# Kernel optimization log

Hardware: AMD Instinct MI355X
Metric: run time of the kernel (lower is better)

Reference implementation:

```python
import math
import jax, jax.numpy as jnp
import numpy as np

DIM = 1536
HEADS = 8
DK = 64
DV = 192
NRPF = 192  # num_rel_pos_features, divisible by 6
SEQ = 1536
BATCH = 4
SCALE = DK ** -0.5


def get_positional_embed(n, feature_size):
    # distances in [-(n-1), n-1], length 2n-1
    dist = jnp.arange(-n + 1, n).astype(jnp.float32)
    adist = jnp.abs(dist)[:, None]  # [2n-1, 1]
    f = feature_size // 6  # 3 feature fns, each doubled by sign channel
    # exponential half-life features
    max_range = math.log(n) / math.log(2.0)
    half_life = 2.0 ** jnp.linspace(3.0, max_range, f)[None, :]
    emb_exp = jnp.exp(-math.log(2.0) / half_life * adist)
    # central mask features
    center_widths = (2.0 ** jnp.arange(1, f + 1).astype(jnp.float32) - 1.0)[None, :]
    emb_cm = (center_widths > adist).astype(jnp.float32)
    # gamma pdf features
    stddev = n / (2.0 * f)
    start_mean = n / float(f)
    mean = jnp.linspace(start_mean, float(n), f)[None, :]
    conc = (mean / stddev) ** 2
    rate = mean / stddev ** 2
    log_unnorm = (conc - 1.0) * jnp.log(jnp.maximum(adist, 1e-20)) - rate * adist
    log_norm = jax.scipy.special.gammaln(conc) - conc * jnp.log(rate)
    prob = jnp.exp(log_unnorm - log_norm) + 1e-8
    emb_g = prob / jnp.max(prob, axis=-1, keepdims=True)
    emb = jnp.concatenate([emb_exp, emb_cm, emb_g], axis=-1)  # [2n-1, feat/2]
    return jnp.concatenate([emb, jnp.sign(dist)[:, None] * emb], axis=-1)  # [2n-1, feat]


def relative_shift(x):
    # x: [b, h, n, 2n-1] -> [b, h, n, n] via the Transformer-XL shift trick
    b, h, t1, t2 = x.shape
    x = jnp.concatenate([jnp.zeros_like(x[..., :1]), x], axis=-1)  # [b,h,t1,t2+1]
    x = x.reshape(b, h, t2 + 1, t1)[:, :, 1:, :].reshape(b, h, t1, t2)
    return x[..., : (t2 + 2) // 2]


def layer_norm(x, g, b, eps=1e-5):
    mu = jnp.mean(x, axis=-1, keepdims=True)
    var = jnp.var(x, axis=-1, keepdims=True)
    return (x - mu) * jax.lax.rsqrt(var + eps) * g + b


def setup_inputs() -> dict:
    key = jax.random.key(0)
    ks = jax.random.split(key, 16)
    d, h, dk, dv = DIM, HEADS, DK, DV
    inp = {
        "x": jax.random.normal(ks[0], (BATCH, SEQ, d), dtype=jnp.float32),
        "ln1_g": jnp.ones((d,), jnp.float32),
        "ln1_b": jnp.zeros((d,), jnp.float32),
        "Wq": jax.random.normal(ks[1], (d, h * dk), jnp.float32) / math.sqrt(d),
        "Wk": jax.random.normal(ks[2], (d, h * dk), jnp.float32) / math.sqrt(d),
        "Wv": jax.random.normal(ks[3], (d, h * dv), jnp.float32) / math.sqrt(d),
        "Wo": jax.random.normal(ks[4], (h * dv, d), jnp.float32) / math.sqrt(h * dv),
        "bo": jnp.zeros((d,), jnp.float32),
        "Wrk": jax.random.normal(ks[5], (NRPF, h * dk), jnp.float32) / math.sqrt(NRPF),
        "rel_content_bias": jax.random.normal(ks[6], (1, h, 1, dk), jnp.float32),
        "rel_pos_bias": jax.random.normal(ks[7], (1, h, 1, dk), jnp.float32),
        "ln2_g": jnp.ones((d,), jnp.float32),
        "ln2_b": jnp.zeros((d,), jnp.float32),
        "W1": jax.random.normal(ks[8], (d, 2 * d), jnp.float32) / math.sqrt(d),
        "b1": jnp.zeros((2 * d,), jnp.float32),
        "W2": jax.random.normal(ks[9], (2 * d, d), jnp.float32) / math.sqrt(2 * d),
        "b2": jnp.zeros((d,), jnp.float32),
    }
    return inp


def _attention(x, Wq, Wk, Wv, Wo, bo, Wrk, rel_content_bias, rel_pos_bias):
    b, n, _ = x.shape
    h, dk, dv = HEADS, DK, DV
    q = (x @ Wq).reshape(b, n, h, dk).transpose(0, 2, 1, 3) * SCALE  # [b,h,n,dk]
    k = (x @ Wk).reshape(b, n, h, dk).transpose(0, 2, 1, 3)
    v = (x @ Wv).reshape(b, n, h, dv).transpose(0, 2, 1, 3)
    content_logits = jnp.einsum('bhid,bhjd->bhij', q + rel_content_bias, k)
    positions = get_positional_embed(n, NRPF)  # [2n-1, NRPF]
    rel_k = (positions @ Wrk).reshape(2 * n - 1, h, dk).transpose(1, 0, 2)  # [h,2n-1,dk]
    rel_logits = jnp.einsum('bhid,hjd->bhij', q + rel_pos_bias, rel_k)
    rel_logits = relative_shift(rel_logits)  # [b,h,n,n]
    attn = jax.nn.softmax(content_logits + rel_logits, axis=-1)
    out = jnp.einsum('bhij,bhjd->bhid', attn, v)
    out = out.transpose(0, 2, 1, 3).reshape(b, n, h * dv)
    return out @ Wo + bo


def reference(x, ln1_g, ln1_b, Wq, Wk, Wv, Wo, bo, Wrk, rel_content_bias,
              rel_pos_bias, ln2_g, ln2_b, W1, b1, W2, b2):
    # pre-LN attention with residual
    x = x + _attention(layer_norm(x, ln1_g, ln1_b), Wq, Wk, Wv, Wo, bo, Wrk,
                       rel_content_bias, rel_pos_bias)
    # MLP block (carries its own LayerNorm and residual)
    y = layer_norm(x, ln2_g, ln2_b)
    y = jax.nn.relu(y @ W1 + b1)
    y = y @ W2 + b2
    return y + x
```

## Files before the change

kernel.cpp:

```cpp
#include <hip/hip_runtime.h>
#include <hip/hip_bf16.h>
#include <math.h>

#define SEQN 1536
#define NH 8
#define MROWS 6144
#define NDIST 3071

typedef __attribute__((ext_vector_type(8))) _Float16 f16x8;
typedef __attribute__((ext_vector_type(4))) _Float16 f16x4;
typedef __attribute__((ext_vector_type(4))) float f32x4;

#define MFMAH(a, b, c) __builtin_amdgcn_mfma_f32_16x16x32_f16(a, b, c, 0, 0, 0)

__device__ __forceinline__ void gl_lds16(const void* g, void* l) {
  __builtin_amdgcn_global_load_lds(
      (const __attribute__((address_space(1))) void*)g,
      (__attribute__((address_space(3))) void*)l, 16, 0, 0);
}

__global__ __launch_bounds__(64) void pos_embed_kernel(float* __restrict__ pos) {
  int row = blockIdx.x;
  int j = threadIdx.x;
  if (j >= 32) return;
  float dist = (float)(row - (SEQN - 1));
  float adist = fabsf(dist);
  float sgn = (dist > 0.f) ? 1.f : (dist < 0.f ? -1.f : 0.f);

  const float max_range = 10.58496250072116f;
  float hl = exp2f(3.0f + ((max_range - 3.0f) / 31.0f) * (float)j);
  float e_exp = expf(-0.6931471805599453f / hl * adist);

  float cw = exp2f((float)(j + 1)) - 1.0f;
  float e_cm = (cw > adist) ? 1.0f : 0.0f;

  float mean = 48.0f * (float)(j + 1);
  float tt = mean / 24.0f;
  float conc = tt * tt;
  float rate = mean / 576.0f;
  float log_unnorm = (conc - 1.0f) * logf(fmaxf(adist, 1e-20f)) - rate * adist;
  float log_norm = lgammaf(conc) - conc * logf(rate);
  float prob = expf(log_unnorm - log_norm) + 1e-8f;
  float mx = prob;
  #pragma unroll
  for (int off = 16; off >= 1; off >>= 1)
    mx = fmaxf(mx, __shfl_xor(mx, off, 32));
  float e_g = prob / mx;

  float* o = pos + (size_t)row * 192;
  o[j] = e_exp;        o[32 + j] = e_cm;        o[64 + j] = e_g;
  o[96 + j] = sgn * e_exp; o[128 + j] = sgn * e_cm; o[160 + j] = sgn * e_g;
}

__global__ __launch_bounds__(512) void relk_kernel(
    const float* __restrict__ pos, const float* __restrict__ Wrk,
    const float* __restrict__ pb, _Float16* __restrict__ rk, float* __restrict__ PR) {
  __shared__ float prow[16][192];
  const int d0 = blockIdx.x * 16;
  const int t = threadIdx.x;
  #pragma unroll
  for (int p = 0; p < 6; ++p) {
    int idx = t + p * 512;
    int r = idx / 192, c = idx - r * 192;
    prow[r][c] = pos[(size_t)(d0 + r) * 192 + c];
  }
  __syncthreads();
  float acc[16];
  #pragma unroll
  for (int r = 0; r < 16; ++r) acc[r] = 0.f;
  #pragma unroll 4
  for (int kk = 0; kk < 192; ++kk) {
    float wv = Wrk[(size_t)kk * 512 + t];
    #pragma unroll
    for (int r = 0; r < 16; ++r) acc[r] = fmaf(prow[r][kk], wv, acc[r]);
  }
  #pragma unroll
  for (int r = 0; r < 16; ++r)
    rk[(size_t)(d0 + r) * 512 + t] = (_Float16)acc[r];
  float pbv = pb[t];
  #pragma unroll
  for (int r = 0; r < 16; ++r) {
    float pv = pbv * acc[r];
    #pragma unroll
    for (int off = 32; off >= 1; off >>= 1) pv += __shfl_xor(pv, off);
    if ((t & 63) == 0 && (d0 + r) < NDIST)
      PR[(size_t)(t >> 6) * NDIST + d0 + r] = pv;
  }
}

__global__ __launch_bounds__(256) void ln_kernel(
    const float* __restrict__ x, const float* __restrict__ g,
    const float* __restrict__ bta, _Float16* __restrict__ oh) {
  const int row = blockIdx.x;
  const int t = threadIdx.x;
  __shared__ float red[4];
  __shared__ float bc[2];
  const float4* xr = (const float4*)(x + (size_t)row * 1536);
  float4 v0 = xr[t];
  float4 v1 = make_float4(0.f, 0.f, 0.f, 0.f);
  if (t < 128) v1 = xr[256 + t];
  float s = v0.x + v0.y + v0.z + v0.w;
  if (t < 128) s += v1.x + v1.y + v1.z + v1.w;
  #pragma unroll
  for (int off = 32; off >= 1; off >>= 1) s += __shfl_xor(s, off);
  if ((t & 63) == 0) red[t >> 6] = s;
  __syncthreads();
  if (t == 0) bc[0] = (red[0] + red[1] + red[2] + red[3]) * (1.f / 1536.f);
  __syncthreads();
  const float mu = bc[0];
  float d, s2 = 0.f;
  d = v0.x - mu; s2 += d * d; d = v0.y - mu; s2 += d * d;
  d = v0.z - mu; s2 += d * d; d = v0.w - mu; s2 += d * d;
  if (t < 128) {
    d = v1.x - mu; s2 += d * d; d = v1.y - mu; s2 += d * d;
    d = v1.z - mu; s2 += d * d; d = v1.w - mu; s2 += d * d;
  }
  #pragma unroll
  for (int off = 32; off >= 1; off >>= 1) s2 += __shfl_xor(s2, off);
  if ((t & 63) == 0) red[t >> 6] = s2;
  __syncthreads();
  if (t == 0) bc[1] = (red[0] + red[1] + red[2] + red[3]) * (1.f / 1536.f);
  __syncthreads();
  const float inv = rsqrtf(bc[1] + 1e-5f);
  const float4* g4 = (const float4*)g;
  const float4* b4 = (const float4*)bta;
  float4 gg = g4[t], bb = b4[t];
  f16x4 hv;
  hv[0] = (_Float16)((v0.x - mu) * inv * gg.x + bb.x);
  hv[1] = (_Float16)((v0.y - mu) * inv * gg.y + bb.y);
  hv[2] = (_Float16)((v0.z - mu) * inv * gg.z + bb.z);
  hv[3] = (_Float16)((v0.w - mu) * inv * gg.w + bb.w);
  *(f16x4*)(oh + (size_t)row * 1536 + t * 4) = hv;
  if (t < 128) {
    gg = g4[256 + t]; bb = b4[256 + t];
    hv[0] = (_Float16)((v1.x - mu) * inv * gg.x + bb.x);
    hv[1] = (_Float16)((v1.y - mu) * inv * gg.y + bb.y);
    hv[2] = (_Float16)((v1.z - mu) * inv * gg.z + bb.z);
    hv[3] = (_Float16)((v1.w - mu) * inv * gg.w + bb.w);
    *(f16x4*)(oh + (size_t)row * 1536 + 1024 + t * 4) = hv;
  }
}

__global__ __launch_bounds__(256) void convw_kernel(
    const float* __restrict__ W, _Float16* __restrict__ Th,
    int N, int K, int KD, int roff, float scale) {
  __shared__ float tile[32][33];
  const int n0 = blockIdx.x * 32, k0 = blockIdx.y * 32;
  const int t = threadIdx.x;
  const int cr = t >> 5;
  const int cc = t & 31;
  #pragma unroll
  for (int p = 0; p < 4; ++p) {
    int r = cr + p * 8;
    tile[r][cc] = W[(size_t)(k0 + r) * N + n0 + cc];
  }
  __syncthreads();
  #pragma unroll
  for (int p = 0; p < 4; ++p) {
    int r = cr + p * 8;
    float v = tile[cc][r] * scale;
    Th[(size_t)(roff + n0 + r) * KD + k0 + cc] = (_Float16)v;
  }
}

template <int EPI, int BNJ, int MW>
__global__ __launch_bounds__(256, MW) void mgemm_kernel(
    const _Float16* __restrict__ A, const _Float16* __restrict__ B,
    float* __restrict__ C, _Float16* __restrict__ Ch,
    _Float16* __restrict__ Kp, _Float16* __restrict__ Vt, float* __restrict__ CKo,
    const float* __restrict__ bias, const float* __restrict__ res,
    int M, int N, int K) {
  constexpr int BN = BNJ * 32;
  __shared__ _Float16 sm[8192 + BN * 64];
  const int t = threadIdx.x;
  const int lane = t & 63;
  const int w = t >> 6;
  const int wm = w >> 1, wn = w & 1;
  const int slab = (M >> 7) >> 3;
  const int xcd = blockIdx.x & 7;
  const int r = blockIdx.x >> 3;
  const int yt = xcd * slab + (r % slab);
  const int xt = r / slab;
  const int m0 = yt * 128, n0 = xt * BN;

  f32x4 acc[4][BNJ];
  #pragma unroll
  for (int i = 0; i < 4; ++i)
    #pragma unroll
    for (int j = 0; j < BNJ; ++j) acc[i][j] = (f32x4){0.f, 0.f, 0.f, 0.f};

  const int srow = t >> 3;
  const int ssl = t & 7;
  const int ss = ssl ^ (srow & 7);
  const int lr = lane & 15;
  const int g = lane >> 4;
  const int kb = lr & 7;

  for (int k0 = 0; k0 < K; k0 += 64) {
    #pragma unroll
    for (int p = 0; p < 4; ++p) {
      int row = srow + p * 32;
      gl_lds16(A + (size_t)(m0 + row) * K + k0 + ss * 8, &sm[row * 64 + ssl * 8]);
    }
    #pragma unroll
    for (int p = 0; p < BN / 32; ++p) {
      int row = srow + p * 32;
      gl_lds16(B + (size_t)(n0 + row) * K + k0 + ss * 8,
               &sm[8192 + row * 64 + ssl * 8]);
    }
    __syncthreads();
    #pragma unroll
    for (int h2 = 0; h2 < 2; ++h2) {
      const int ksl = ((h2 * 4 + g) ^ kb) * 8;
      f16x8 a[4], b[BNJ];
      #pragma unroll
      for (int i = 0; i < 4; ++i)
        a[i] = *(const f16x8*)(&sm[(wm * 64 + i * 16 + lr) * 64 + ksl]);
      #pragma unroll
      for (int j = 0; j < BNJ; ++j)
        b[j] = *(const f16x8*)(&sm[8192 + (wn * BNJ * 16 + j * 16 + lr) * 64 + ksl]);
      #pragma unroll
      for (int i = 0; i < 4; ++i)
        #pragma unroll
        for (int j = 0; j < BNJ; ++j)
          acc[i][j] = MFMAH(a[i], b[j], acc[i][j]);
    }
    __syncthreads();
  }

  const int lq = lane >> 4;
  #pragma unroll
  for (int i = 0; i < 4; ++i) {
    #pragma unroll
    for (int j = 0; j < BNJ; ++j) {
      const int c0 = n0 + wn * BNJ * 16 + j * 16;
      const int col = c0 + lr;
      const int rbase = m0 + wm * 64 + i * 16 + lq * 4;
      if (EPI == 3) {
        #pragma unroll
        for (int q = 0; q < 4; ++q) {
          size_t o = (size_t)(rbase + q) * N + col;
          C[o] = acc[i][j][q] + bias[col] + res[o];
        }
      } else if (EPI == 2) {
        #pragma unroll
        for (int q = 0; q < 4; ++q) {
          size_t o = (size_t)(rbase + q) * N + col;
          Ch[o] = (_Float16)fmaxf(acc[i][j][q] + bias[col], 0.f);
        }
      } else {
        if (c0 < 512) {
          #pragma unroll
          for (int q = 0; q < 4; ++q)
            Ch[(size_t)(rbase + q) * 512 + col] = (_Float16)acc[i][j][q];
        } else if (c0 < 1024) {
          #pragma unroll
          for (int q = 0; q < 4; ++q)
            Kp[(size_t)(rbase + q) * 512 + (col - 512)] = (_Float16)acc[i][j][q];
        } else {
          int dv = col - 1024;
          int hd = dv / 192;
          int dvh = dv - hd * 192;
          int bb = rbase / 1536;
          int nloc = rbase - bb * 1536;
          f16x4 pk;
          pk[0] = (_Float16)acc[i][j][0];
          pk[1] = (_Float16)acc[i][j][1];
          pk[2] = (_Float16)acc[i][j][2];
          pk[3] = (_Float16)acc[i][j][3];
          *(f16x4*)(Vt + (((size_t)bb * 8 + hd) * 192 + dvh) * 1536 + nloc) = pk;
        }
      }
    }
  }

  if (EPI == 4) {
    const int cw0 = n0 + wn * 64;
    if (cw0 >= 512 && cw0 < 1024) {
      const int hh = (cw0 - 512) >> 6;
      float cbv[4];
      #pragma unroll
      for (int j = 0; j < 4; ++j) cbv[j] = bias[cw0 - 512 + j * 16 + lr];
      #pragma unroll
      for (int i = 0; i < 4; ++i)
        #pragma unroll
        for (int q = 0; q < 4; ++q) {
          float v = acc[i][0][q] * cbv[0] + acc[i][1][q] * cbv[1] +
                    acc[i][2][q] * cbv[2] + acc[i][3][q] * cbv[3];
          #pragma unroll
          for (int off = 8; off >= 1; off >>= 1) v += __shfl_xor(v, off);
          if (lr == 0)
            CKo[(size_t)(m0 + wm * 64 + i * 16 + lq * 4 + q) * 8 + hh] = v;
        }
    }
  }
}

__global__ __launch_bounds__(256, 3) void attn_kernel(
    const _Float16* __restrict__ Qp, const _Float16* __restrict__ Kp,
    const _Float16* __restrict__ Vt, const _Float16* __restrict__ rk,
    const float* __restrict__ PR, const float* __restrict__ CK,
    _Float16* __restrict__ ao) {
  __shared__ _Float16 lds[26752];
  const int id = blockIdx.x;
  const int xcd = id & 7, s = id >> 3;
  const int bh = xcd * 4 + s / 24;
  const int it = s % 24;
  const int b = bh >> 3, h = bh & 7;
  const int t = threadIdx.x;
  const int w = t >> 6;
  const int lane = t & 63;
  const int c15 = lane & 15, g = lane >> 4;
  const int swz = c15 & 7;
  const int vsz = (c15 >> 1) & 3;
  const int qrow0 = it * 64 + w * 16;
  const int rrow0 = 48 - w * 16;
  const int R0 = 1472 - it * 64;

  const int lr = lane >> 3, sl = lane & 7;
  const int ss = sl ^ lr;
  const int ss2 = (lane & 3) ^ ((lane >> 3) & 3);

  f16x8 qh0, qh1;
  {
    size_t qo = ((size_t)(b * SEQN + qrow0 + c15)) * 512 + h * 64 + g * 8;
    qh0 = *(const f16x8*)(Qp + qo);
    qh1 = *(const f16x8*)(Qp + qo + 32);
  }
  f16x8 ones;
  #pragma unroll
  for (int i = 0; i < 8; ++i) ones[i] = (_Float16)1.0f;

  const int klA = c15 * 64 + ((g ^ swz)) * 8;
  const int klB = c15 * 64 + (((4 + g) ^ swz)) * 8;
  const int vl  = c15 * 32 + ((g ^ vsz)) * 8;
  const int pwr = 24576 + (w * 16 + 4 * g) * 34 + c15;
  const int pfr = 24576 + (w * 16 + c15) * 34 + g * 8;

  const _Float16* kg = Kp + ((size_t)(b * SEQN) + 32 + w * 8 + lr) * 512 + h * 64 + ss * 8;
  const _Float16* vg = Vt + (((size_t)(b * 8 + h)) * 192 + w * 48 + (lane >> 2)) * SEQN + 32 + ss2 * 8;
  const _Float16* rg = rk + ((size_t)(R0 + 96) + w * 8 + lr) * 512 + h * 64 + ss * 8;
  const float* prg = PR + (size_t)h * NDIST + 1520 - qrow0 + c15;
  const float* ckg = CK + (size_t)b * SEQN * 8 + h + c15 * 8;

  f32x4 acc[13];
  #pragma unroll
  for (int d = 0; d < 13; ++d) acc[d] = (f32x4){0.f, 0.f, 0.f, 0.f};
  float mrun[4];
  #pragma unroll
  for (int q = 0; q < 4; ++q) mrun[q] = -1e30f;

  {
    size_t gk = ((size_t)(b * SEQN) + w * 8 + lr) * 512 + h * 64 + ss * 8;
    gl_lds16(Kp + gk, &lds[w * 512]);
    #pragma unroll
    for (int p = 0; p < 3; ++p) {
      size_t gv = (((size_t)(b * 8 + h)) * 192 + w * 48 + p * 16 + (lane >> 2)) * SEQN + ss2 * 8;
      gl_lds16(Vt + gv, &lds[4096 + (w * 48 + p * 16) * 32]);
    }
    #pragma unroll
    for (int p = 0; p < 4; ++p) {
      int rr = w * 32 + p * 8 + lr;
      size_t gr = ((size_t)(R0 + rr)) * 512 + h * 64 + ss * 8;
      gl_lds16(rk + gr, &lds[16384 + (w * 32 + p * 8) * 64]);
    }
  }

  f32x4 T0, T1, T2;

  #define COMP_T(DST, ETOFF)                                                    \
    do {                                                                        \
      int relrow = (cc32 + rrow0 + (ETOFF) + c15) & 127;                        \
      f16x8 r0_ = *(const f16x8*)(&lds[16384 + relrow * 64 + ((g ^ swz)) * 8]); \
      f16x8 r1_ = *(const f16x8*)(&lds[16384 + relrow * 64 + (((4 + g) ^ swz)) * 8]); \
      f32x4 tt_ = (f32x4){0.f, 0.f, 0.f, 0.f};                                  \
      tt_ = MFMAH(qh0, r0_, tt_);                                               \
      tt_ = MFMAH(qh1, r1_, tt_);                                               \
      float prv_ = prg[(ETOFF)];                                                \
      _Pragma("unroll") for (int q = 0; q < 4; ++q) tt_[q] += prv_;             \
      DST = tt_;                                                                \
    } while (0)

  #define CHUNK_BODY(CIDX, P)                                                   \
  {                                                                             \
    const int c = (CIDX);                                                       \
    const int cc32 = c * 32;                                                    \
    constexpr int KB = (P) * 2048;                                              \
    constexpr int VB = 4096 + (P) * 6144;                                       \
    constexpr int KBn = (1 - (P)) * 2048;                                       \
    constexpr int VBn = 4096 + (1 - (P)) * 6144;                                \
    __syncthreads();  \
    if (c < 47) {                                                               \
      gl_lds16(kg, &lds[KBn + w * 512]);                                        \
      gl_lds16(vg, &lds[VBn + (w * 48) * 32]);                                  \
      gl_lds16(vg + (size_t)16 * SEQN, &lds[VBn + (w * 48 + 16) * 32]);         \
      gl_lds16(vg + (size_t)32 * SEQN, &lds[VBn + (w * 48 + 32) * 32]);         \
      if (c >= 1) {                                                             \
        int dr = ((cc32 + 96 + w * 8) & 127) * 64;                              \
        gl_lds16(rg, &lds[16384 + dr]);                                         \
      }                                                                         \
    }                                                                           \
    __builtin_amdgcn_s_setprio(1);                                              \
    if (c == 0) { COMP_T(T0, 0); } else { T0 = T2; }                            \
    COMP_T(T1, 16);                                                             \
    COMP_T(T2, 32);                                                             \
    f32x4 S[2];                                                                 \
    _Pragma("unroll") for (int st = 0; st < 2; ++st) {                          \
      f16x8 kh0 = *(const f16x8*)(&lds[KB + st * 1024 + klA]);                  \
      f16x8 kh1 = *(const f16x8*)(&lds[KB + st * 1024 + klB]);                  \
      f32x4 ssv = (f32x4){0.f, 0.f, 0.f, 0.f};                                  \
      ssv = MFMAH(qh0, kh0, ssv);                                               \
      ssv = MFMAH(qh1, kh1, ssv);                                               \
      S[st] = ssv;                                                              \
    }                                                                           \
    __builtin_amdgcn_s_setprio(0);                                              \
    float ck0 = ckg[0];                                                         \
    float ck1 = ckg[128];                                                       \
    _Pragma("unroll") for (int q = 0; q < 4; ++q) {                             \
      int eoff = c15 + 15 - 4 * g - q;                                          \
      int src = (lane & 48) | (eoff & 15);                                      \
      float t0v = __shfl(T0[q], src);                                           \
      float t1v = __shfl(T1[q], src);                                           \
      float t2v = __shfl(T2[q], src);                                           \
      bool lo = eoff < 16;                                                      \
      S[0][q] += ck0 + (lo ? t0v : t1v);                                        \
      S[1][q] += ck1 + (lo ? t1v : t2v);                                        \
    }                                                                           \
    int need = 0;                                                               \
    _Pragma("unroll") for (int st = 0; st < 2; ++st)                            \
      _Pragma("unroll") for (int q = 0; q < 4; ++q)                             \
        need |= (S[st][q] > mrun[q] + 8.0f) ? 1 : 0;                            \
    if (__any(need)) {                                                          \
      float mx[4];                                                              \
      _Pragma("unroll") for (int q = 0; q < 4; ++q)                             \
        mx[q] = fmaxf(S[0][q], S[1][q]);                                        \
      _Pragma("unroll") for (int off = 8; off >= 1; off >>= 1)                  \
        _Pragma("unroll") for (int q = 0; q < 4; ++q)                           \
          mx[q] = fmaxf(mx[q], __shfl_xor(mx[q], off));                         \
      _Pragma("unroll") for (int q = 0; q < 4; ++q) {                           \
        float mn = fmaxf(mrun[q], mx[q]);                                       \
        float al = __expf(mrun[q] - mn);                                        \
        mrun[q] = mn;                                                           \
        _Pragma("unroll") for (int d = 0; d < 13; ++d) acc[d][q] *= al;         \
      }                                                                         \
    }                                                                           \
    _Pragma("unroll") for (int st = 0; st < 2; ++st)                            \
      _Pragma("unroll") for (int q = 0; q < 4; ++q)                             \
        lds[pwr + q * 34 + st * 16] = (_Float16)__expf(S[st][q] - mrun[q]);     \
    f16x8 pf = *(const f16x8*)(&lds[pfr]);                                      \
    __builtin_amdgcn_s_setprio(1);                                              \
    _Pragma("unroll") for (int d = 0; d < 12; ++d) {                            \
      f16x8 vf = *(const f16x8*)(&lds[VB + d * 512 + vl]);                      \
      acc[d] = MFMAH(pf, vf, acc[d]);                                           \
    }                                                                           \
    acc[12] = MFMAH(pf, ones, acc[12]);                                         \
    __builtin_amdgcn_s_setprio(0);                                              \
    kg += 32 * 512;                                                             \
    vg += 32;                                                                   \
    rg += 32 * 512;                                                             \
    prg += 32;                                                                  \
    ckg += 256;                                                                 \
  }

  for (int cc = 0; cc < 48; cc += 2) {
    CHUNK_BODY(cc, 0);
    CHUNK_BODY(cc + 1, 1);
  }
  #undef CHUNK_BODY
  #undef COMP_T

  float rinv[4];
  #pragma unroll
  for (int q = 0; q < 4; ++q) rinv[q] = 1.0f / acc[12][q];
  #pragma unroll
  for (int d = 0; d < 12; ++d) {
    int col = h * 192 + d * 16 + c15;
    #pragma unroll
    for (int q = 0; q < 4; ++q) {
      size_t row = (size_t)(b * SEQN + qrow0 + 4 * g + q);
      ao[row * 1536 + col] = (_Float16)(acc[d][q] * rinv[q]);
    }
  }
}

extern "C" void kernel_launch(void* const* d_in, const int* in_sizes, int n_in,
                              void* d_out, int out_size, void* d_ws, size_t ws_size,
                              hipStream_t stream) {
  (void)in_sizes; (void)n_in; (void)out_size; (void)ws_size;
  const float* x   = (const float*)d_in[0];
  const float* g1  = (const float*)d_in[1];
  const float* be1 = (const float*)d_in[2];
  const float* Wq  = (const float*)d_in[3];
  const float* Wk  = (const float*)d_in[4];
  const float* Wv  = (const float*)d_in[5];
  const float* Wo  = (const float*)d_in[6];
  const float* bo  = (const float*)d_in[7];
  const float* Wrk = (const float*)d_in[8];
  const float* cb  = (const float*)d_in[9];
  const float* pb  = (const float*)d_in[10];
  const float* g2  = (const float*)d_in[11];
  const float* be2 = (const float*)d_in[12];
  const float* W1  = (const float*)d_in[13];
  const float* b1  = (const float*)d_in[14];
  const float* W2  = (const float*)d_in[15];
  const float* b2  = (const float*)d_in[16];
  float* out = (float*)d_out;

  char* B = (char*)d_ws;
  float* pos     = (float*)(B + 0);
  _Float16* rk   = (_Float16*)(B + 2359296);
  float* PRb     = (float*)(B + 5505024);
  float* CKb     = (float*)(B + 5603328);
  _Float16* xn   = (_Float16*)(B + 5799936);
  _Float16* Wb   = (_Float16*)(B + 24674304);
  _Float16* Qp   = (_Float16*)(B + 34111488);
  _Float16* Kp   = (_Float16*)(B + 40402944);
  _Float16* Vtp  = (_Float16*)(B + 46694400);
  _Float16* ao   = (_Float16*)(B + 65568768);
  float* x2      = (float*)(B + 84443136);
  _Float16* h1   = (_Float16*)(B + 122191872);

  pos_embed_kernel<<<NDIST, 64, 0, stream>>>(pos);
  relk_kernel<<<192, 512, 0, stream>>>(pos, Wrk, pb, rk, PRb);
  ln_kernel<<<MROWS, 256, 0, stream>>>(x, g1, be1, xn);
  convw_kernel<<<dim3(16, 48), 256, 0, stream>>>(Wq, Wb, 512, 1536, 1536, 0, 0.125f);
  convw_kernel<<<dim3(16, 48), 256, 0, stream>>>(Wk, Wb, 512, 1536, 1536, 512, 1.0f);
  convw_kernel<<<dim3(48, 48), 256, 0, stream>>>(Wv, Wb, 1536, 1536, 1536, 1024, 1.0f);
  mgemm_kernel<4, 4, 4><<<960, 256, 0, stream>>>(
      xn, Wb, nullptr, Qp, Kp, Vtp, CKb, cb, nullptr, MROWS, 2560, 1536);
  attn_kernel<<<768, 256, 0, stream>>>(Qp, Kp, Vtp, rk, PRb, CKb, ao);
  convw_kernel<<<dim3(48, 48), 256, 0, stream>>>(Wo, Wb, 1536, 1536, 1536, 0, 1.0f);
  mgemm_kernel<3, 3, 4><<<768, 256, 0, stream>>>(
      ao, Wb, x2, nullptr, nullptr, nullptr, nullptr, bo, x, MROWS, 1536, 1536);
  ln_kernel<<<MROWS, 256, 0, stream>>>(x2, g2, be2, xn);
  convw_kernel<<<dim3(96, 48), 256, 0, stream>>>(W1, Wb, 3072, 1536, 1536, 0, 1.0f);
  mgemm_kernel<2, 6, 3><<<768, 256, 0, stream>>>(
      xn, Wb, nullptr, h1, nullptr, nullptr, nullptr, b1, nullptr, MROWS, 3072, 1536);
  convw_kernel<<<dim3(48, 96), 256, 0, stream>>>(W2, Wb, 1536, 3072, 3072, 0, 1.0f);
  mgemm_kernel<3, 3, 4><<<768, 256, 0, stream>>>(
      h1, Wb, out, nullptr, nullptr, nullptr, nullptr, b2, x2, MROWS, 1536, 3072);
}
```

Before: 420.2 us.

## Load relative-key fragments straight into registers and drop the LDS ring buffer

Removes the 128-row relative-key ring buffer from shared memory. Each wave now loads its rel_k MFMA fragments directly from global memory into registers, prefetched one chunk ahead. This shrinks the LDS footprint so the launch bound can rise from 3 to 4 blocks per CU for more occupancy. In exchange, global reads become uncoalesced per-lane 16-byte loads that may be fetched redundantly across waves, and register pressure rises under the tighter launch bound.

Measured after the change: 797.5 us. 1.9x slower.

```diff
diff --git a/kernel.cpp b/kernel.cpp
--- a/kernel.cpp
+++ b/kernel.cpp
@@ -296,12 +296,12 @@
   }
 }
 
-__global__ __launch_bounds__(256, 3) void attn_kernel(
+__global__ __launch_bounds__(256, 4) void attn_kernel(
     const _Float16* __restrict__ Qp, const _Float16* __restrict__ Kp,
     const _Float16* __restrict__ Vt, const _Float16* __restrict__ rk,
     const float* __restrict__ PR, const float* __restrict__ CK,
     _Float16* __restrict__ ao) {
-  __shared__ _Float16 lds[26752];
+  __shared__ _Float16 lds[18560];
   const int id = blockIdx.x;
   const int xcd = id & 7, s = id >> 3;
   const int bh = xcd * 4 + s / 24;
@@ -334,14 +334,14 @@
   const int klA = c15 * 64 + ((g ^ swz)) * 8;
   const int klB = c15 * 64 + (((4 + g) ^ swz)) * 8;
   const int vl  = c15 * 32 + ((g ^ vsz)) * 8;
-  const int pwr = 24576 + (w * 16 + 4 * g) * 34 + c15;
-  const int pfr = 24576 + (w * 16 + c15) * 34 + g * 8;
+  const int pwr = 16384 + (w * 16 + 4 * g) * 34 + c15;
+  const int pfr = 16384 + (w * 16 + c15) * 34 + g * 8;
 
   const _Float16* kg = Kp + ((size_t)(b * SEQN) + 32 + w * 8 + lr) * 512 + h * 64 + ss * 8;
   const _Float16* vg = Vt + (((size_t)(b * 8 + h)) * 192 + w * 48 + (lane >> 2)) * SEQN + 32 + ss2 * 8;
-  const _Float16* rg = rk + ((size_t)(R0 + 96) + w * 8 + lr) * 512 + h * 64 + ss * 8;
   const float* prg = PR + (size_t)h * NDIST + 1520 - qrow0 + c15;
   const float* ckg = CK + (size_t)b * SEQN * 8 + h + c15 * 8;
+  const _Float16* rgp = rk + ((size_t)(R0 + rrow0 + c15)) * 512 + h * 64 + g * 8;
 
   f32x4 acc[13];
   #pragma unroll
@@ -358,24 +358,22 @@
       size_t gv = (((size_t)(b * 8 + h)) * 192 + w * 48 + p * 16 + (lane >> 2)) * SEQN + ss2 * 8;
       gl_lds16(Vt + gv, &lds[4096 + (w * 48 + p * 16) * 32]);
     }
-    #pragma unroll
-    for (int p = 0; p < 4; ++p) {
-      int rr = w * 32 + p * 8 + lr;
-      size_t gr = ((size_t)(R0 + rr)) * 512 + h * 64 + ss * 8;
-      gl_lds16(rk + gr, &lds[16384 + (w * 32 + p * 8) * 64]);
-    }
-  }
+  }
+  f16x8 r00 = *(const f16x8*)(rgp);
+  f16x8 r01 = *(const f16x8*)(rgp + 32);
+  f16x8 rA0 = *(const f16x8*)(rgp + 16 * 512);
+  f16x8 rA1 = *(const f16x8*)(rgp + 16 * 512 + 32);
+  f16x8 rB0 = *(const f16x8*)(rgp + 32 * 512);
+  f16x8 rB1 = *(const f16x8*)(rgp + 32 * 512 + 32);
+  rgp += 48 * 512;
 
   f32x4 T0, T1, T2;
 
-  #define COMP_T(DST, ETOFF)                                                    \
+  #define COMP_T_REG(DST, RH0, RH1, ETOFF)                                      \
     do {                                                                        \
-      int relrow = (cc32 + rrow0 + (ETOFF) + c15) & 127;                        \
-      f16x8 r0_ = *(const f16x8*)(&lds[16384 + relrow * 64 + ((g ^ swz)) * 8]); \
-      f16x8 r1_ = *(const f16x8*)(&lds[16384 + relrow * 64 + (((4 + g) ^ swz)) * 8]); \
       f32x4 tt_ = (f32x4){0.f, 0.f, 0.f, 0.f};                                  \
-      tt_ = MFMAH(qh0, r0_, tt_);                                               \
-      tt_ = MFMAH(qh1, r1_, tt_);                                               \
+      tt_ = MFMAH(qh0, RH0, tt_);                                               \
+      tt_ = MFMAH(qh1, RH1, tt_);                                               \
       float prv_ = prg[(ETOFF)];                                                \
       _Pragma("unroll") for (int q = 0; q < 4; ++q) tt_[q] += prv_;             \
       DST = tt_;                                                                \
@@ -384,7 +382,6 @@
   #define CHUNK_BODY(CIDX, P)                                                   \
   {                                                                             \
     const int c = (CIDX);                                                       \
-    const int cc32 = c * 32;                                                    \
     constexpr int KB = (P) * 2048;                                              \
     constexpr int VB = 4096 + (P) * 6144;                                       \
     constexpr int KBn = (1 - (P)) * 2048;                                       \
@@ -395,15 +392,11 @@
       gl_lds16(vg, &lds[VBn + (w * 48) * 32]);                                  \
       gl_lds16(vg + (size_t)16 * SEQN, &lds[VBn + (w * 48 + 16) * 32]);         \
       gl_lds16(vg + (size_t)32 * SEQN, &lds[VBn + (w * 48 + 32) * 32]);         \
-      if (c >= 1) {                                                             \
-        int dr = ((cc32 + 96 + w * 8) & 127) * 64;                              \
-        gl_lds16(rg, &lds[16384 + dr]);                                         \
-      }                                                                         \
     }                                                                           \
     __builtin_amdgcn_s_setprio(1);                                              \
-    if (c == 0) { COMP_T(T0, 0); } else { T0 = T2; }                            \
-    COMP_T(T1, 16);                                                             \
-    COMP_T(T2, 32);                                                             \
+    if (c == 0) { COMP_T_REG(T0, r00, r01, 0); } else { T0 = T2; }              \
+    COMP_T_REG(T1, rA0, rA1, 16);                                               \
+    COMP_T_REG(T2, rB0, rB1, 32);                                               \
     f32x4 S[2];                                                                 \
     _Pragma("unroll") for (int st = 0; st < 2; ++st) {                          \
       f16x8 kh0 = *(const f16x8*)(&lds[KB + st * 1024 + klA]);                  \
@@ -414,6 +407,13 @@
       S[st] = ssv;                                                              \
     }                                                                           \
     __builtin_amdgcn_s_setprio(0);                                              \
+    if (c < 47) {                   \
+      rA0 = *(const f16x8*)(rgp);                                               \
+      rA1 = *(const f16x8*)(rgp + 32);                                          \
+      rB0 = *(const f16x8*)(rgp + 16 * 512);                                    \
+      rB1 = *(const f16x8*)(rgp + 16 * 512 + 32);                               \
+      rgp += 32 * 512;                                                          \
+    }                                                                           \
     float ck0 = ckg[0];                                                         \
     float ck1 = ckg[128];                                                       \
     _Pragma("unroll") for (int q = 0; q < 4; ++q) {                             \
@@ -457,7 +457,6 @@
     __builtin_amdgcn_s_setprio(0);                                              \
     kg += 32 * 512;                                                             \
     vg += 32;                                                                   \
-    rg += 32 * 512;                                                             \
     prg += 32;                                                                  \
     ckg += 256;                                                                 \
   }
@@ -467,7 +466,7 @@
     CHUNK_BODY(cc + 1, 1);
   }
   #undef CHUNK_BODY
-  #undef COMP_T
+  #undef COMP_T_REG
 
   float rinv[4];
   #pragma unroll
```
